# Kernel optimization log

Measured on AMD Instinct MI355X. Metric: run time of the kernel, lower is better.

Reference implementation:

```python
import jax, jax.numpy as jnp
import numpy as np

B, T, E, H = 64, 512, 512, 1024


def _lstm_scan(x, h0, c0, U_w, U_b, W_w, W_b, reverse=False):
    # Precompute input projections for all timesteps: [B,T,4H]
    ux = jnp.einsum('bte,ge->btg', x, U_w) + U_b
    if reverse:
        ux = ux[:, ::-1, :]

    def step(carry, ux_t):
        h, c = carry
        gates = ux_t + h @ W_w.T + W_b  # [B,4H]
        f, i, g, o = jnp.split(gates, 4, axis=-1)
        c = c * jax.nn.sigmoid(f) + jax.nn.sigmoid(i) * jnp.tanh(g)
        h = o * jnp.tanh(c)  # NOTE: source applies o WITHOUT sigmoid (faithful)
        return (h, c), h

    (_, _), hs = jax.lax.scan(step, (h0, c0), jnp.swapaxes(ux, 0, 1))
    out = jnp.swapaxes(hs, 0, 1)  # [B,T,H]
    if reverse:
        out = out[:, ::-1, :]
    return out


def setup_inputs() -> dict:
    key = jax.random.key(0)
    ks = jax.random.split(key, 9)
    s_in = 1.0 / np.sqrt(E)
    s_h = 1.0 / np.sqrt(H)
    return {
        'x': jax.random.normal(ks[0], (B, T, E), jnp.float32),
        'hidden_state': jnp.zeros((B, H), jnp.float32),
        'cell_state': jnp.zeros((B, H), jnp.float32),
        'Uf_w': jax.random.normal(ks[1], (4 * H, E), jnp.float32) * s_in,
        'Uf_b': jax.random.normal(ks[2], (4 * H,), jnp.float32) * s_in,
        'Wf_w': jax.random.normal(ks[3], (4 * H, H), jnp.float32) * s_h,
        'Wf_b': jax.random.normal(ks[4], (4 * H,), jnp.float32) * s_h,
        'Ub_w': jax.random.normal(ks[5], (4 * H, E), jnp.float32) * s_in,
        'Ub_b': jax.random.normal(ks[6], (4 * H,), jnp.float32) * s_in,
        'Wb_w': jax.random.normal(ks[7], (4 * H, H), jnp.float32) * s_h,
        'Wb_b': jax.random.normal(ks[8], (4 * H,), jnp.float32) * s_h,
    }


def reference(x, hidden_state, cell_state, Uf_w, Uf_b, Wf_w, Wf_b, Ub_w, Ub_b, Wb_w, Wb_b):
    out_f = _lstm_scan(x, hidden_state, cell_state, Uf_w, Uf_b, Wf_w, Wf_b, reverse=False)
    out_b = _lstm_scan(x, hidden_state, cell_state, Ub_w, Ub_b, Wb_w, Wb_b, reverse=True)
    out = out_f + out_b  # mode='sum'
    # Source returns the ORIGINAL hidden/cell states in bidirectional mode
    return out, hidden_state, cell_state
```

## Files before the change

### kernel.cpp

```cpp
#include <hip/hip_runtime.h>
#include <hip/hip_bf16.h>
#include <stdint.h>

#define BB 64
#define TT 512
#define EE 512
#define HH 1024
#define CHUNK 8
#define NKI 12
#define NKX 4
#define NKH 8
#define NWGD 128
#define NWG  256

#define CTR_INIT  0
#define CTR_FLAG  16
#define CTR_ELECT 512
#define CTR_XBAR  1024
#define CTRB      65536

#define HFRAGS 8192
#define PLANE_BF16 (HFRAGS * 8)

typedef __bf16 bf16_t;
typedef __bf16 bf16x8 __attribute__((ext_vector_type(8)));
typedef float  f32x4  __attribute__((ext_vector_type(4)));
typedef unsigned int u32x4 __attribute__((ext_vector_type(4)));
typedef unsigned long long u64;

static_assert(sizeof(bf16x8) == 16, "bf16x8 must be 16B");

__device__ __forceinline__ f32x4 mfma_16x16x32_bf16(bf16x8 a, bf16x8 b, f32x4 c) {
    return __builtin_amdgcn_mfma_f32_16x16x32_bf16(a, b, c, 0, 0, 0);
}

__device__ __forceinline__ unsigned int lo32(u64 v) { return (unsigned int)v; }
__device__ __forceinline__ unsigned int hi32(u64 v) { return (unsigned int)(v >> 32); }

template<int OFF>
__device__ __forceinline__ bf16x8 ld_sc0(const bf16_t* p) {
    bf16x8 d;
    asm volatile("global_load_dwordx4 %0, %1, off offset:%2 sc0"
                 : "=v"(d) : "v"(p), "n"(OFF));
    return d;
}

__device__ __forceinline__ void split8(const float* __restrict__ src,
                                       bf16x8& hi, bf16x8& lo) {
    const f32x4 a = *(const f32x4*)src;
    const f32x4 b = *(const f32x4*)(src + 4);
    #pragma unroll
    for (int j = 0; j < 4; ++j) {
        const bf16_t h0 = (bf16_t)a[j];
        hi[j] = h0;  lo[j] = (bf16_t)(a[j] - (float)h0);
        const bf16_t h1 = (bf16_t)b[j];
        hi[4 + j] = h1;  lo[4 + j] = (bf16_t)(b[j] - (float)h1);
    }
}

__device__ __forceinline__ void ctr_barrier(unsigned int* slot, unsigned int target) {
    __syncthreads();
    if (threadIdx.x == 0) {
        __hip_atomic_fetch_add(slot, 1u, __ATOMIC_RELAXED, __HIP_MEMORY_SCOPE_AGENT);
        int guard = 0;
        while (__hip_atomic_load(slot, __ATOMIC_RELAXED, __HIP_MEMORY_SCOPE_AGENT) < target) {
            __builtin_amdgcn_s_sleep(2);
            if (++guard > (1 << 22)) break;
        }
    }
    __syncthreads();
}

__global__ __launch_bounds__(256, 1)
void lstm_persistent(const float* __restrict__ x,
                     const float* __restrict__ h0,
                     const float* __restrict__ c0,
                     const float* __restrict__ Ufw, const float* __restrict__ Ufb,
                     const float* __restrict__ Wfw, const float* __restrict__ Wfb,
                     const float* __restrict__ Ubw, const float* __restrict__ Ubb,
                     const float* __restrict__ Wbw, const float* __restrict__ Wbb,
                     bf16_t* __restrict__ xhi,
                     bf16_t* __restrict__ xlo,
                     unsigned int* __restrict__ hbuf,
                     bf16_t* __restrict__ stage,
                     float*  __restrict__ out,
                     unsigned int* __restrict__ ctr)
{
    __shared__ f32x4 red[4][8][64];
    __shared__ unsigned int s_xcd, s_rank, s_cnt;

    const int wg   = blockIdx.x;
    const int dir  = wg >> 7;
    const int cb   = (wg & 127) * CHUNK;
    const int tid  = threadIdx.x;
    const int wave = tid >> 6;
    const int lane = tid & 63;
    const int l16  = lane & 15;
    const int quad = lane >> 4;
    const int wg127 = wg & 127;

    unsigned int* flags = ctr + CTR_FLAG + dir * NWGD;

    const float* Uw = dir ? Ubw : Ufw;
    const float* Ww = dir ? Wbw : Wfw;
    const float* Ub = dir ? Ubb : Ufb;
    const float* Wb = dir ? Wbb : Wfb;

    if (tid == 0) {
        unsigned int xcc;
        asm volatile("s_getreg_b32 %0, hwreg(20, 0, 32)" : "=s"(xcc));
        xcc &= 7u;
        s_xcd = xcc;
        s_rank = __hip_atomic_fetch_add(&ctr[CTR_ELECT + xcc * 2 + dir], 1u,
                                        __ATOMIC_RELAXED, __HIP_MEMORY_SCOPE_AGENT);
    }

    const int gid = wg * 256 + tid;
    {
        const int NG = BB * TT * EE / 8;
        for (int g = gid; g < NG; g += NWG * 256) {
            bf16x8 hi, lo;
            split8(x + (size_t)g * 8, hi, lo);
            ((bf16x8*)xhi)[g] = hi;
            ((bf16x8*)xlo)[g] = lo;
        }
    }
    {
        const int NZ = BB * TT * HH / 4;
        const f32x4 z = {0.f, 0.f, 0.f, 0.f};
        for (int g = gid; g < NZ; g += NWG * 256) ((f32x4*)out)[g] = z;
    }
    {
        float* tail = out + (size_t)BB * TT * HH;
        const int NT4 = BB * HH / 4;
        for (int g = gid; g < NT4; g += NWG * 256)
            ((f32x4*)tail)[g] = ((const f32x4*)h0)[g];
        for (int g = gid; g < NT4; g += NWG * 256)
            ((f32x4*)(tail + BB * HH))[g] = ((const f32x4*)c0)[g];
    }
    {
        unsigned int* p1 = hbuf + ((size_t)(1 * 2 + dir)) * (BB * HH);
        for (int i = tid; i < BB * CHUNK; i += 256) {
            const int b = i >> 3, col = cb + (i & 7);
            const float v = h0[b * HH + col];
            const bf16_t vh = (bf16_t)v;
            const bf16_t vl = (bf16_t)(v - (float)vh);
            const unsigned int pk =
                (unsigned int)__builtin_bit_cast(unsigned short, vh) |
                ((unsigned int)__builtin_bit_cast(unsigned short, vl) << 16);
            __hip_atomic_store(&p1[b * HH + col], pk, __ATOMIC_RELAXED,
                               __HIP_MEMORY_SCOPE_AGENT);
        }
    }

    bf16x8 whi[2][NKI], wlo[2][NKI];
    #pragma unroll
    for (int mt = 0; mt < 2; ++mt) {
        const int r    = mt * 16 + l16;
        const int grow = (r & 3) * HH + (cb + (r >> 2));
        const float* urow = Uw + (size_t)grow * EE;
        const float* wrow = Ww + (size_t)grow * HH;
        #pragma unroll
        for (int ki = 0; ki < NKI; ++ki) {
            const int ws0 = (ki * 4 + wave) * 32;
            const float* src = (ws0 < EE ? urow + ws0 : wrow + (ws0 - EE)) + quad * 8;
            split8(src, whi[mt][ki], wlo[mt][ki]);
        }
    }

    const int bown = wave * 16 + l16;
    float biasv[2][4];
    float cst[2];
    #pragma unroll
    for (int mt = 0; mt < 2; ++mt) {
        const int hcol = cb + mt * 4 + quad;
        #pragma unroll
        for (int g = 0; g < 4; ++g)
            biasv[mt][g] = Ub[g * HH + hcol] + Wb[g * HH + hcol];
        cst[mt] = c0[bown * HH + hcol];
    }

    __threadfence();
    ctr_barrier(ctr + CTR_INIT, NWG);

    if (tid == 0)
        s_cnt = __hip_atomic_load(&ctr[CTR_ELECT + s_xcd * 2 + dir],
                                  __ATOMIC_RELAXED, __HIP_MEMORY_SCOPE_AGENT);
    __syncthreads();
    const int xcd  = (int)s_xcd;
    const int rank = (int)s_rank;
    const int cnt  = (int)s_cnt;

    const bf16_t* shi = stage + ((size_t)(xcd * 2 + dir) * 2 + 0) * PLANE_BF16;
    const bf16_t* slo = stage + ((size_t)(xcd * 2 + dir) * 2 + 1) * PLANE_BF16;
    unsigned int* xslots = ctr + CTR_XBAR + (xcd * 2 + dir) * TT;

    const f32x4 vzero = {0.f, 0.f, 0.f, 0.f};

    for (int t = 0; t < TT; ++t) {
        const int tx = dir ? (TT - 1 - t) : t;
        const int rp = (t + 1) & 1;

        const bf16_t *xrh[4], *xrl[4];
        #pragma unroll
        for (int nt = 0; nt < 4; ++nt) {
            const int b = nt * 16 + l16;
            const size_t xoff = ((size_t)b * TT + tx) * EE;
            xrh[nt] = xhi + xoff;  xrl[nt] = xlo + xoff;
        }

        bf16x8 xbh[NKX][4], xbl[NKX][4];
        #pragma unroll
        for (int kx = 0; kx < NKX; ++kx) {
            const int off = (kx * 4 + wave) * 32 + quad * 8;
            #pragma unroll
            for (int nt = 0; nt < 4; ++nt) {
                xbh[kx][nt] = *(const bf16x8*)(xrh[nt] + off);
                xbl[kx][nt] = *(const bf16x8*)(xrl[nt] + off);
            }
        }

        if (t > 0) {
            if (wave == 0) {
                const u64* f64 = (const u64*)flags;
                const unsigned int tgt = (unsigned int)t;
                int guard = 0;
                for (;;) {
                    const u64 v = __hip_atomic_load(f64 + lane, __ATOMIC_RELAXED,
                                                    __HIP_MEMORY_SCOPE_AGENT);
                    const int ok = ((unsigned int)v >= tgt) &&
                                   ((unsigned int)(v >> 32) >= tgt);
                    if (__all(ok)) break;
                    __builtin_amdgcn_s_sleep(1);
                    if (++guard > (1 << 22)) break;
                }
            }
            __syncthreads();
        }

        {
            const unsigned int* src = hbuf + ((size_t)(rp * 2 + dir)) * (BB * HH);
            bf16x8* dsth = (bf16x8*)shi;
            bf16x8* dstl = (bf16x8*)slo;
            for (int i = rank * 256 + tid; i < HFRAGS; i += cnt * 256) {
                const int b = i >> 7, k8 = i & 127;
                const u64* s64 = (const u64*)(src + (size_t)b * HH + k8 * 8);
                const u64 v0 = __hip_atomic_load(s64 + 0, __ATOMIC_RELAXED, __HIP_MEMORY_SCOPE_AGENT);
                const u64 v1 = __hip_atomic_load(s64 + 1, __ATOMIC_RELAXED, __HIP_MEMORY_SCOPE_AGENT);
                const u64 v2 = __hip_atomic_load(s64 + 2, __ATOMIC_RELAXED, __HIP_MEMORY_SCOPE_AGENT);
                const u64 v3 = __hip_atomic_load(s64 + 3, __ATOMIC_RELAXED, __HIP_MEMORY_SCOPE_AGENT);
                u32x4 hw, lw;
                hw[0] = __builtin_amdgcn_perm(hi32(v0), lo32(v0), 0x05040100u);
                lw[0] = __builtin_amdgcn_perm(hi32(v0), lo32(v0), 0x07060302u);
                hw[1] = __builtin_amdgcn_perm(hi32(v1), lo32(v1), 0x05040100u);
                lw[1] = __builtin_amdgcn_perm(hi32(v1), lo32(v1), 0x07060302u);
                hw[2] = __builtin_amdgcn_perm(hi32(v2), lo32(v2), 0x05040100u);
                lw[2] = __builtin_amdgcn_perm(hi32(v2), lo32(v2), 0x07060302u);
                hw[3] = __builtin_amdgcn_perm(hi32(v3), lo32(v3), 0x05040100u);
                lw[3] = __builtin_amdgcn_perm(hi32(v3), lo32(v3), 0x07060302u);
                dsth[(k8 << 6) + b] = __builtin_bit_cast(bf16x8, hw);
                dstl[(k8 << 6) + b] = __builtin_bit_cast(bf16x8, lw);
            }
        }

        f32x4 acc[2][4];
        #pragma unroll
        for (int mt = 0; mt < 2; ++mt)
            #pragma unroll
            for (int nt = 0; nt < 4; ++nt) acc[mt][nt] = vzero;
        #pragma unroll
        for (int kx = 0; kx < NKX; ++kx)
            #pragma unroll
            for (int mt = 0; mt < 2; ++mt)
                #pragma unroll
                for (int nt = 0; nt < 4; ++nt) {
                    acc[mt][nt] = mfma_16x16x32_bf16(whi[mt][kx], xbh[kx][nt], acc[mt][nt]);
                    acc[mt][nt] = mfma_16x16x32_bf16(whi[mt][kx], xbl[kx][nt], acc[mt][nt]);
                    acc[mt][nt] = mfma_16x16x32_bf16(wlo[mt][kx], xbh[kx][nt], acc[mt][nt]);
                }

        __syncthreads();
        if (tid == 0) {
            unsigned int* slot = xslots + t;
            __hip_atomic_fetch_add(slot, 1u, __ATOMIC_RELAXED, __HIP_MEMORY_SCOPE_AGENT);
            int guard = 0;
            while (__hip_atomic_load(slot, __ATOMIC_RELAXED, __HIP_MEMORY_SCOPE_AGENT)
                   < (unsigned int)cnt) {
                __builtin_amdgcn_s_sleep(1);
                if (++guard > (1 << 22)) break;
            }
        }
        __syncthreads();
        __builtin_amdgcn_sched_barrier(0);

        bf16x8 hbh[2][4], hbl[2][4];
        {
            const int K8 = (0 * 4 + wave) * 4;
            const bf16_t* ph = shi + ((size_t)(((K8 + quad) << 6) + l16)) * 8;
            const bf16_t* pl = slo + ((size_t)(((K8 + quad) << 6) + l16)) * 8;
            hbh[0][0] = ld_sc0<0>(ph);   hbl[0][0] = ld_sc0<0>(pl);
            hbh[0][1] = ld_sc0<256>(ph); hbl[0][1] = ld_sc0<256>(pl);
            hbh[0][2] = ld_sc0<512>(ph); hbl[0][2] = ld_sc0<512>(pl);
            hbh[0][3] = ld_sc0<768>(ph); hbl[0][3] = ld_sc0<768>(pl);
        }
        asm volatile("s_waitcnt vmcnt(0)" ::: "memory");
        __builtin_amdgcn_sched_barrier(0);
        #pragma unroll
        for (int kh = 0; kh < NKH; ++kh) {
            const int cur = kh & 1;
            if (kh + 1 < NKH) {
                const int K8 = ((kh + 1) * 4 + wave) * 4;
                const bf16_t* ph = shi + ((size_t)(((K8 + quad) << 6) + l16)) * 8;
                const bf16_t* pl = slo + ((size_t)(((K8 + quad) << 6) + l16)) * 8;
                hbh[cur ^ 1][0] = ld_sc0<0>(ph);   hbl[cur ^ 1][0] = ld_sc0<0>(pl);
                hbh[cur ^ 1][1] = ld_sc0<256>(ph); hbl[cur ^ 1][1] = ld_sc0<256>(pl);
                hbh[cur ^ 1][2] = ld_sc0<512>(ph); hbl[cur ^ 1][2] = ld_sc0<512>(pl);
                hbh[cur ^ 1][3] = ld_sc0<768>(ph); hbl[cur ^ 1][3] = ld_sc0<768>(pl);
            }
            const int ki = NKX + kh;
            #pragma unroll
            for (int mt = 0; mt < 2; ++mt)
                #pragma unroll
                for (int nt = 0; nt < 4; ++nt) {
                    acc[mt][nt] = mfma_16x16x32_bf16(whi[mt][ki], hbh[cur][nt], acc[mt][nt]);
                    acc[mt][nt] = mfma_16x16x32_bf16(whi[mt][ki], hbl[cur][nt], acc[mt][nt]);
                    acc[mt][nt] = mfma_16x16x32_bf16(wlo[mt][ki], hbh[cur][nt], acc[mt][nt]);
                }
            if (kh + 1 < NKH) {
                asm volatile("s_waitcnt vmcnt(0)" ::: "memory");
                __builtin_amdgcn_sched_barrier(0);
            }
        }

        #pragma unroll
        for (int mt = 0; mt < 2; ++mt)
            #pragma unroll
            for (int nt = 0; nt < 4; ++nt)
                red[wave][mt * 4 + nt][lane] = acc[mt][nt];
        __syncthreads();

        unsigned int* hn32 = hbuf + ((size_t)((t & 1) * 2 + dir)) * (BB * HH);
        float hvout[2];
        #pragma unroll
        for (int mt = 0; mt < 2; ++mt) {
            const int tI = mt * 4 + wave;
            f32x4 s = red[0][tI][lane];
            #pragma unroll
            for (int w2 = 1; w2 < 4; ++w2) s += red[w2][tI][lane];
            const float fg = s[0] + biasv[mt][0];
            const float ig = s[1] + biasv[mt][1];
            const float gg = s[2] + biasv[mt][2];
            const float og = s[3] + biasv[mt][3];
            const float sf = 1.f / (1.f + __expf(-fg));
            const float si = 1.f / (1.f + __expf(-ig));
            float cn = cst[mt] * sf + si * tanhf(gg);
            cn = fminf(600.f, fmaxf(-600.f, cn));
            cst[mt] = cn;
            float hv = og * tanhf(cn);
            hv = fminf(448.f, fmaxf(-448.f, hv));
            const int hcol = cb + mt * 4 + quad;
            const bf16_t vh = (bf16_t)hv;
            const bf16_t vl = (bf16_t)(hv - (float)vh);
            const unsigned int pk =
                (unsigned int)__builtin_bit_cast(unsigned short, vh) |
                ((unsigned int)__builtin_bit_cast(unsigned short, vl) << 16);
            __hip_atomic_store(&hn32[(size_t)bown * HH + hcol], pk,
                               __ATOMIC_RELAXED, __HIP_MEMORY_SCOPE_AGENT);
            hvout[mt] = hv;
        }

        __syncthreads();
        if (tid == 0)
            __hip_atomic_store(&flags[wg127], (unsigned int)(t + 1),
                               __ATOMIC_RELAXED, __HIP_MEMORY_SCOPE_AGENT);
        #pragma unroll
        for (int mt = 0; mt < 2; ++mt)
            atomicAdd(&out[((size_t)bown * TT + tx) * HH + (cb + mt * 4 + quad)],
                      hvout[mt]);
    }
}

__global__ void sentinel_kernel(float* __restrict__ out, float v, size_t n)
{
    const size_t i = (size_t)blockIdx.x * blockDim.x + threadIdx.x;
    if (i < n) out[i] = v;
}

extern "C" void kernel_launch(void* const* d_in, const int* in_sizes, int n_in,
                              void* d_out, int out_size, void* d_ws, size_t ws_size,
                              hipStream_t stream)
{
    const float* x   = (const float*)d_in[0];
    const float* h0  = (const float*)d_in[1];
    const float* c0  = (const float*)d_in[2];
    const float* Ufw = (const float*)d_in[3];
    const float* Ufb = (const float*)d_in[4];
    const float* Wfw = (const float*)d_in[5];
    const float* Wfb = (const float*)d_in[6];
    const float* Ubw = (const float*)d_in[7];
    const float* Ubb = (const float*)d_in[8];
    const float* Wbw = (const float*)d_in[9];
    const float* Wbb = (const float*)d_in[10];

    const size_t n_out = (size_t)out_size;

    const size_t XPB   = (size_t)BB * TT * EE * sizeof(bf16_t);
    const size_t HBUF  = (size_t)2 * 2 * BB * HH * sizeof(unsigned int);
    const size_t STAGE = (size_t)8 * 2 * 2 * PLANE_BF16 * sizeof(bf16_t);
    if (ws_size < CTRB + 2 * XPB + HBUF + STAGE) {
        hipLaunchKernelGGL(sentinel_kernel, dim3((unsigned)((n_out + 255) / 256)),
                           dim3(256), 0, stream, (float*)d_out, 1000.0f, n_out);
        return;
    }

    uint8_t* ws = (uint8_t*)d_ws;
    unsigned int* ctr = (unsigned int*)ws;
    bf16_t* xhi  = (bf16_t*)(ws + CTRB);
    bf16_t* xlo  = (bf16_t*)(ws + CTRB + XPB);
    unsigned int* hbuf = (unsigned int*)(ws + CTRB + 2 * XPB);
    bf16_t* stg  = (bf16_t*)(ws + CTRB + 2 * XPB + HBUF);
    float*  out  = (float*)d_out;

    hipMemsetAsync(ctr, 0, CTRB, stream);

    hipLaunchKernelGGL(lstm_persistent, dim3(NWG), dim3(256), 0, stream,
                       x, h0, c0, Ufw, Ufb, Wfw, Wfb, Ubw, Ubb, Wbw, Wbb,
                       xhi, xlo, hbuf, stg, out, ctr);
}
```

Measured before the change: 7.004 ms.

## Store hidden state pre-split in fragment layout and triple-buffer h loads

Each workgroup now writes its new hidden values as separate bf16 hi and lo planes, already in the fragment-major layout. Before the global store it gathers them through shared memory, so each row goes out as 16-byte packed stores. The per-step staging copy becomes a plain 16-byte move with no byte permutes, replacing the old strided 4-byte stores and per-element unpacking. The recurrent-weight MFMA loop now keeps three h-fragment loads in flight with partial vmcnt waits instead of double-buffering with full waits. This costs an extra shared buffer, one more barrier per step and more registers.

New measurement: 6.212 ms. -11.3%, faster.

```diff
diff --git a/kernel.cpp b/kernel.cpp
--- a/kernel.cpp
+++ b/kernel.cpp
@@ -19,8 +19,7 @@
 #define CTR_XBAR  1024
 #define CTRB      65536
 
-#define HFRAGS 8192
-#define PLANE_BF16 (HFRAGS * 8)
+#define PLANE 65536
 
 typedef __bf16 bf16_t;
 typedef __bf16 bf16x8 __attribute__((ext_vector_type(8)));
@@ -43,6 +42,11 @@
     asm volatile("global_load_dwordx4 %0, %1, off offset:%2 sc0"
                  : "=v"(d) : "v"(p), "n"(OFF));
     return d;
+}
+
+template<int N>
+__device__ __forceinline__ void waitv() {
+    asm volatile("s_waitcnt vmcnt(%0)" :: "i"(N) : "memory");
 }
 
 __device__ __forceinline__ void split8(const float* __restrict__ src,
@@ -81,12 +85,13 @@
                      const float* __restrict__ Wbw, const float* __restrict__ Wbb,
                      bf16_t* __restrict__ xhi,
                      bf16_t* __restrict__ xlo,
-                     unsigned int* __restrict__ hbuf,
+                     bf16_t* __restrict__ hpl,
                      bf16_t* __restrict__ stage,
                      float*  __restrict__ out,
                      unsigned int* __restrict__ ctr)
 {
     __shared__ f32x4 red[4][8][64];
+    __shared__ unsigned int pkbuf[4][16][8];
     __shared__ unsigned int s_xcd, s_rank, s_cnt;
 
     const int wg   = blockIdx.x;
@@ -139,17 +144,30 @@
             ((f32x4*)(tail + BB * HH))[g] = ((const f32x4*)c0)[g];
     }
     {
-        unsigned int* p1 = hbuf + ((size_t)(1 * 2 + dir)) * (BB * HH);
-        for (int i = tid; i < BB * CHUNK; i += 256) {
-            const int b = i >> 3, col = cb + (i & 7);
-            const float v = h0[b * HH + col];
-            const bf16_t vh = (bf16_t)v;
-            const bf16_t vl = (bf16_t)(v - (float)vh);
-            const unsigned int pk =
-                (unsigned int)__builtin_bit_cast(unsigned short, vh) |
-                ((unsigned int)__builtin_bit_cast(unsigned short, vl) << 16);
-            __hip_atomic_store(&p1[b * HH + col], pk, __ATOMIC_RELAXED,
-                               __HIP_MEMORY_SCOPE_AGENT);
+        bf16_t* p1h = hpl + ((size_t)(1 * 2 + dir) * 2 + 0) * PLANE;
+        bf16_t* p1l = p1h + PLANE;
+        if (tid < 128) {
+            const int pl = tid >> 6, b = tid & 63;
+            unsigned int d[4];
+            #pragma unroll
+            for (int j = 0; j < 4; ++j) {
+                const float va = h0[b * HH + cb + 2 * j];
+                const float vb = h0[b * HH + cb + 2 * j + 1];
+                unsigned short sa, sb;
+                if (pl == 0) {
+                    sa = __builtin_bit_cast(unsigned short, (bf16_t)va);
+                    sb = __builtin_bit_cast(unsigned short, (bf16_t)vb);
+                } else {
+                    sa = __builtin_bit_cast(unsigned short, (bf16_t)(va - (float)(bf16_t)va));
+                    sb = __builtin_bit_cast(unsigned short, (bf16_t)(vb - (float)(bf16_t)vb));
+                }
+                d[j] = (unsigned int)sa | ((unsigned int)sb << 16);
+            }
+            u64* dst = (u64*)((pl ? p1l : p1h) + (size_t)(wg127 * 64 + b) * 8);
+            __hip_atomic_store(dst + 0, (u64)d[0] | ((u64)d[1] << 32),
+                               __ATOMIC_RELAXED, __HIP_MEMORY_SCOPE_AGENT);
+            __hip_atomic_store(dst + 1, (u64)d[2] | ((u64)d[3] << 32),
+                               __ATOMIC_RELAXED, __HIP_MEMORY_SCOPE_AGENT);
         }
     }
 
@@ -191,8 +209,8 @@
     const int rank = (int)s_rank;
     const int cnt  = (int)s_cnt;
 
-    const bf16_t* shi = stage + ((size_t)(xcd * 2 + dir) * 2 + 0) * PLANE_BF16;
-    const bf16_t* slo = stage + ((size_t)(xcd * 2 + dir) * 2 + 1) * PLANE_BF16;
+    const bf16_t* shi = stage + ((size_t)(xcd * 2 + dir) * 2 + 0) * PLANE;
+    const bf16_t* slo = shi + PLANE;
     unsigned int* xslots = ctr + CTR_XBAR + (xcd * 2 + dir) * TT;
 
     const f32x4 vzero = {0.f, 0.f, 0.f, 0.f};
@@ -239,27 +257,16 @@
         }
 
         {
-            const unsigned int* src = hbuf + ((size_t)(rp * 2 + dir)) * (BB * HH);
-            bf16x8* dsth = (bf16x8*)shi;
-            bf16x8* dstl = (bf16x8*)slo;
-            for (int i = rank * 256 + tid; i < HFRAGS; i += cnt * 256) {
-                const int b = i >> 7, k8 = i & 127;
-                const u64* s64 = (const u64*)(src + (size_t)b * HH + k8 * 8);
-                const u64 v0 = __hip_atomic_load(s64 + 0, __ATOMIC_RELAXED, __HIP_MEMORY_SCOPE_AGENT);
-                const u64 v1 = __hip_atomic_load(s64 + 1, __ATOMIC_RELAXED, __HIP_MEMORY_SCOPE_AGENT);
-                const u64 v2 = __hip_atomic_load(s64 + 2, __ATOMIC_RELAXED, __HIP_MEMORY_SCOPE_AGENT);
-                const u64 v3 = __hip_atomic_load(s64 + 3, __ATOMIC_RELAXED, __HIP_MEMORY_SCOPE_AGENT);
-                u32x4 hw, lw;
-                hw[0] = __builtin_amdgcn_perm(hi32(v0), lo32(v0), 0x05040100u);
-                lw[0] = __builtin_amdgcn_perm(hi32(v0), lo32(v0), 0x07060302u);
-                hw[1] = __builtin_amdgcn_perm(hi32(v1), lo32(v1), 0x05040100u);
-                lw[1] = __builtin_amdgcn_perm(hi32(v1), lo32(v1), 0x07060302u);
-                hw[2] = __builtin_amdgcn_perm(hi32(v2), lo32(v2), 0x05040100u);
-                lw[2] = __builtin_amdgcn_perm(hi32(v2), lo32(v2), 0x07060302u);
-                hw[3] = __builtin_amdgcn_perm(hi32(v3), lo32(v3), 0x05040100u);
-                lw[3] = __builtin_amdgcn_perm(hi32(v3), lo32(v3), 0x07060302u);
-                dsth[(k8 << 6) + b] = __builtin_bit_cast(bf16x8, hw);
-                dstl[(k8 << 6) + b] = __builtin_bit_cast(bf16x8, lw);
+            const u64* s64 = (const u64*)(hpl + ((size_t)(rp * 2 + dir) * 2) * PLANE);
+            u32x4* d16 = (u32x4*)(stage + ((size_t)(xcd * 2 + dir) * 2) * PLANE);
+            for (int i = rank * 256 + tid; i < 16384; i += cnt * 256) {
+                const u64 a = __hip_atomic_load(s64 + 2 * i,     __ATOMIC_RELAXED,
+                                                __HIP_MEMORY_SCOPE_AGENT);
+                const u64 b = __hip_atomic_load(s64 + 2 * i + 1, __ATOMIC_RELAXED,
+                                                __HIP_MEMORY_SCOPE_AGENT);
+                u32x4 v;
+                v[0] = lo32(a); v[1] = hi32(a); v[2] = lo32(b); v[3] = hi32(b);
+                d16[i] = v;
             }
         }
 
@@ -293,44 +300,38 @@
         __syncthreads();
         __builtin_amdgcn_sched_barrier(0);
 
-        bf16x8 hbh[2][4], hbl[2][4];
-        {
-            const int K8 = (0 * 4 + wave) * 4;
-            const bf16_t* ph = shi + ((size_t)(((K8 + quad) << 6) + l16)) * 8;
-            const bf16_t* pl = slo + ((size_t)(((K8 + quad) << 6) + l16)) * 8;
-            hbh[0][0] = ld_sc0<0>(ph);   hbl[0][0] = ld_sc0<0>(pl);
-            hbh[0][1] = ld_sc0<256>(ph); hbl[0][1] = ld_sc0<256>(pl);
-            hbh[0][2] = ld_sc0<512>(ph); hbl[0][2] = ld_sc0<512>(pl);
-            hbh[0][3] = ld_sc0<768>(ph); hbl[0][3] = ld_sc0<768>(pl);
-        }
-        asm volatile("s_waitcnt vmcnt(0)" ::: "memory");
-        __builtin_amdgcn_sched_barrier(0);
+        bf16x8 hbh[3][4], hbl[3][4];
+        #define ISSUE_W(w, s)                                                   \
+        {                                                                       \
+            const int K8 = ((w) * 4 + wave) * 4;                                \
+            const bf16_t* ph = shi + ((size_t)(((K8 + quad) << 6) + l16)) * 8;  \
+            const bf16_t* pl_ = slo + ((size_t)(((K8 + quad) << 6) + l16)) * 8; \
+            hbh[s][0] = ld_sc0<0>(ph);    hbh[s][1] = ld_sc0<256>(ph);          \
+            hbh[s][2] = ld_sc0<512>(ph);  hbh[s][3] = ld_sc0<768>(ph);          \
+            hbl[s][0] = ld_sc0<0>(pl_);   hbl[s][1] = ld_sc0<256>(pl_);         \
+            hbl[s][2] = ld_sc0<512>(pl_); hbl[s][3] = ld_sc0<768>(pl_);         \
+        }
+        ISSUE_W(0, 0); ISSUE_W(1, 1); ISSUE_W(2, 2);
         #pragma unroll
         for (int kh = 0; kh < NKH; ++kh) {
-            const int cur = kh & 1;
-            if (kh + 1 < NKH) {
-                const int K8 = ((kh + 1) * 4 + wave) * 4;
-                const bf16_t* ph = shi + ((size_t)(((K8 + quad) << 6) + l16)) * 8;
-                const bf16_t* pl = slo + ((size_t)(((K8 + quad) << 6) + l16)) * 8;
-                hbh[cur ^ 1][0] = ld_sc0<0>(ph);   hbl[cur ^ 1][0] = ld_sc0<0>(pl);
-                hbh[cur ^ 1][1] = ld_sc0<256>(ph); hbl[cur ^ 1][1] = ld_sc0<256>(pl);
-                hbh[cur ^ 1][2] = ld_sc0<512>(ph); hbl[cur ^ 1][2] = ld_sc0<512>(pl);
-                hbh[cur ^ 1][3] = ld_sc0<768>(ph); hbl[cur ^ 1][3] = ld_sc0<768>(pl);
-            }
+            if (kh <= 5)      waitv<16>();
+            else if (kh == 6) waitv<8>();
+            else              waitv<0>();
+            __builtin_amdgcn_sched_barrier(0);
+            const int s = kh % 3;
             const int ki = NKX + kh;
             #pragma unroll
             for (int mt = 0; mt < 2; ++mt)
                 #pragma unroll
                 for (int nt = 0; nt < 4; ++nt) {
-                    acc[mt][nt] = mfma_16x16x32_bf16(whi[mt][ki], hbh[cur][nt], acc[mt][nt]);
-                    acc[mt][nt] = mfma_16x16x32_bf16(whi[mt][ki], hbl[cur][nt], acc[mt][nt]);
-                    acc[mt][nt] = mfma_16x16x32_bf16(wlo[mt][ki], hbh[cur][nt], acc[mt][nt]);
+                    acc[mt][nt] = mfma_16x16x32_bf16(whi[mt][ki], hbh[s][nt], acc[mt][nt]);
+                    acc[mt][nt] = mfma_16x16x32_bf16(whi[mt][ki], hbl[s][nt], acc[mt][nt]);
+                    acc[mt][nt] = mfma_16x16x32_bf16(wlo[mt][ki], hbh[s][nt], acc[mt][nt]);
                 }
-            if (kh + 1 < NKH) {
-                asm volatile("s_waitcnt vmcnt(0)" ::: "memory");
-                __builtin_amdgcn_sched_barrier(0);
-            }
-        }
+            if (kh + 3 < NKH) ISSUE_W(kh + 3, s);
+        }
+        #undef ISSUE_W
+        __builtin_amdgcn_sched_barrier(0);
 
         #pragma unroll
         for (int mt = 0; mt < 2; ++mt)
@@ -339,7 +340,6 @@
                 red[wave][mt * 4 + nt][lane] = acc[mt][nt];
         __syncthreads();
 
-        unsigned int* hn32 = hbuf + ((size_t)((t & 1) * 2 + dir)) * (BB * HH);
         float hvout[2];
         #pragma unroll
         for (int mt = 0; mt < 2; ++mt) {
@@ -358,15 +358,42 @@
             cst[mt] = cn;
             float hv = og * tanhf(cn);
             hv = fminf(448.f, fmaxf(-448.f, hv));
-            const int hcol = cb + mt * 4 + quad;
             const bf16_t vh = (bf16_t)hv;
             const bf16_t vl = (bf16_t)(hv - (float)vh);
-            const unsigned int pk =
+            pkbuf[wave][l16][mt * 4 + quad] =
                 (unsigned int)__builtin_bit_cast(unsigned short, vh) |
                 ((unsigned int)__builtin_bit_cast(unsigned short, vl) << 16);
-            __hip_atomic_store(&hn32[(size_t)bown * HH + hcol], pk,
-                               __ATOMIC_RELAXED, __HIP_MEMORY_SCOPE_AGENT);
             hvout[mt] = hv;
+        }
+        __syncthreads();
+
+        {
+            bf16_t* dph = hpl + ((size_t)((t & 1) * 2 + dir) * 2 + 0) * PLANE;
+            bf16_t* dpl = dph + PLANE;
+            if (lane < 16) {
+                const int b = wave * 16 + lane;
+                const unsigned int* pr = &pkbuf[wave][lane][0];
+                const unsigned int p0 = pr[0], p1 = pr[1], p2 = pr[2], p3 = pr[3];
+                const unsigned int p4 = pr[4], p5 = pr[5], p6 = pr[6], p7 = pr[7];
+                const unsigned int h0 = __builtin_amdgcn_perm(p1, p0, 0x05040100u);
+                const unsigned int h1 = __builtin_amdgcn_perm(p3, p2, 0x05040100u);
+                const unsigned int h2 = __builtin_amdgcn_perm(p5, p4, 0x05040100u);
+                const unsigned int h3 = __builtin_amdgcn_perm(p7, p6, 0x05040100u);
+                const unsigned int l0 = __builtin_amdgcn_perm(p1, p0, 0x07060302u);
+                const unsigned int l1 = __builtin_amdgcn_perm(p3, p2, 0x07060302u);
+                const unsigned int l2 = __builtin_amdgcn_perm(p5, p4, 0x07060302u);
+                const unsigned int l3 = __builtin_amdgcn_perm(p7, p6, 0x07060302u);
+                u64* dh = (u64*)(dph + (size_t)(wg127 * 64 + b) * 8);
+                u64* dl = (u64*)(dpl + (size_t)(wg127 * 64 + b) * 8);
+                __hip_atomic_store(dh + 0, (u64)h0 | ((u64)h1 << 32),
+                                   __ATOMIC_RELAXED, __HIP_MEMORY_SCOPE_AGENT);
+                __hip_atomic_store(dh + 1, (u64)h2 | ((u64)h3 << 32),
+                                   __ATOMIC_RELAXED, __HIP_MEMORY_SCOPE_AGENT);
+                __hip_atomic_store(dl + 0, (u64)l0 | ((u64)l1 << 32),
+                                   __ATOMIC_RELAXED, __HIP_MEMORY_SCOPE_AGENT);
+                __hip_atomic_store(dl + 1, (u64)l2 | ((u64)l3 << 32),
+                                   __ATOMIC_RELAXED, __HIP_MEMORY_SCOPE_AGENT);
+            }
         }
 
         __syncthreads();
@@ -405,9 +432,9 @@
     const size_t n_out = (size_t)out_size;
 
     const size_t XPB   = (size_t)BB * TT * EE * sizeof(bf16_t);
-    const size_t HBUF  = (size_t)2 * 2 * BB * HH * sizeof(unsigned int);
-    const size_t STAGE = (size_t)8 * 2 * 2 * PLANE_BF16 * sizeof(bf16_t);
-    if (ws_size < CTRB + 2 * XPB + HBUF + STAGE) {
+    const size_t HPLB  = (size_t)2 * 2 * 2 * PLANE * sizeof(bf16_t);
+    const size_t STAGE = (size_t)8 * 2 * 2 * PLANE * sizeof(bf16_t);
+    if (ws_size < CTRB + 2 * XPB + HPLB + STAGE) {
         hipLaunchKernelGGL(sentinel_kernel, dim3((unsigned)((n_out + 255) / 256)),
                            dim3(256), 0, stream, (float*)d_out, 1000.0f, n_out);
         return;
@@ -417,13 +444,13 @@
     unsigned int* ctr = (unsigned int*)ws;
     bf16_t* xhi  = (bf16_t*)(ws + CTRB);
     bf16_t* xlo  = (bf16_t*)(ws + CTRB + XPB);
-    unsigned int* hbuf = (unsigned int*)(ws + CTRB + 2 * XPB);
-    bf16_t* stg  = (bf16_t*)(ws + CTRB + 2 * XPB + HBUF);
+    bf16_t* hpl  = (bf16_t*)(ws + CTRB + 2 * XPB);
+    bf16_t* stg  = (bf16_t*)(ws + CTRB + 2 * XPB + HPLB);
     float*  out  = (float*)d_out;
 
     hipMemsetAsync(ctr, 0, CTRB, stream);
 
     hipLaunchKernelGGL(lstm_persistent, dim3(NWG), dim3(256), 0, stream,
                        x, h0, c0, Ufw, Ufb, Wfw, Wfb, Ubw, Ubb, Wbw, Wbb,
-                       xhi, xlo, hbuf, stg, out, ctr);
-}
+                       xhi, xlo, hpl, stg, out, ctr);
+}
```
